# Kernel tuning notes

Measured on AMD Instinct MI355X. Metric: run time of the kernel, lower is better.

The kernel has to match this reference:

```python
import jax, jax.numpy as jnp
import numpy as np

B, H, T, K, V = 2, 8, 2048, 128, 128


def setup_inputs() -> dict:
    key = jax.random.key(0)
    k1, k2, k3, k4, k5 = jax.random.split(key, 5)
    return {
        "q": jax.random.normal(k1, (B, H, T, K), dtype=jnp.float32),
        "k": jax.random.normal(k2, (B, H, T, K), dtype=jnp.float32),
        "v": jax.random.normal(k3, (B, H, T, V), dtype=jnp.float32),
        "i_gate": jax.random.normal(k4, (B, H, T), dtype=jnp.float32),
        "f_gate": jax.random.normal(k5, (B, H, T), dtype=jnp.float32),
    }


def reference(q, k, v, i_gate, f_gate):
    # Stabilized parallel mLSTM (same math as the chunked Triton kernel,
    # expressed in natural-log base instead of base-2).
    Bq, Hq, Tq, Kd = q.shape
    scale = Kd ** -0.5
    logf = jax.nn.log_sigmoid(f_gate)                      # [B,H,T]
    fc = jnp.cumsum(logf, axis=-1)                         # cumulative forget logits
    # log decay matrix: logD[t,s] = i[s] + (fc[t] - fc[s]) for s <= t
    logD = fc[..., :, None] - fc[..., None, :] + i_gate[..., None, :]  # [B,H,T,T]
    mask = jnp.tril(jnp.ones((Tq, Tq), dtype=bool))
    logD_masked = jnp.where(mask, logD, -jnp.inf)
    m = jnp.max(logD_masked, axis=-1)                      # row-wise stabilizer [B,H,T]
    D = jnp.where(mask, jnp.exp(logD - m[..., None]), 0.0) # stabilized decay matrix
    S = jnp.einsum("bhtk,bhsk->bhts", q, k) * scale * D    # gated scores
    norm = jnp.maximum(jnp.abs(jnp.sum(S, axis=-1)), jnp.exp(-m))  # [B,H,T]
    h = jnp.einsum("bhts,bhsv->bhtv", S, v) / norm[..., None]
    return h
```

## Files before the change

kernel.cpp:

```cpp
#include <hip/hip_runtime.h>

#define T_SEQ 2048
#define DHEAD 128
#define NBH 16
#define SCALE 0.08838834764831845f

typedef unsigned short u16;
typedef unsigned int u32;
typedef u16 u16x4 __attribute__((ext_vector_type(4)));
typedef u16 u16x8 __attribute__((ext_vector_type(8)));
typedef u32 u32x2 __attribute__((ext_vector_type(2)));
typedef short s16x4 __attribute__((ext_vector_type(4)));
typedef __bf16 bf16x8 __attribute__((ext_vector_type(8)));
typedef float f32x4 __attribute__((ext_vector_type(4)));

__device__ __forceinline__ u16 f2bfu(float x) {
  union { float f; unsigned u; } c; c.f = x;
  unsigned u = c.u;
  u = u + 0x7FFFu + ((u >> 16) & 1u);
  return (u16)(u >> 16);
}

__device__ __forceinline__ bf16x8 ldsFrag(const u16* p) {
  u16x8 t = *(const u16x8*)p;
  return __builtin_bit_cast(bf16x8, t);
}

__device__ __forceinline__ f32x4 mfma16x16x16bf16(s16x4 a, s16x4 b, f32x4 c) {
#if __has_builtin(__builtin_amdgcn_mfma_f32_16x16x16bf16_1k)
  return __builtin_amdgcn_mfma_f32_16x16x16bf16_1k(a, b, c, 0, 0, 0);
#else
  asm("v_mfma_f32_16x16x16_bf16 %0, %1, %2, %0" : "+v"(c) : "v"(a), "v"(b));
  return c;
#endif
}

__global__ __launch_bounds__(1024) void gate_scan_kernel(
    const float* __restrict__ ig, const float* __restrict__ fg,
    float* __restrict__ a_out, float* __restrict__ c_out,
    float* __restrict__ fc_out)
{
  const int bh = blockIdx.x, tid = threadIdx.x;
  const int w = tid >> 6, lane = tid & 63;
  const int base = bh * T_SEQ + tid * 2;
  __shared__ float wsum[16];
  __shared__ float wmax[16];

  const float x0 = fg[base], x1 = fg[base + 1];
  const float ls0 = fminf(x0, 0.f) - log1pf(expf(-fabsf(x0)));
  const float ls1 = fminf(x1, 0.f) - log1pf(expf(-fabsf(x1)));
  const float s = ls0 + ls1;

  float sc = s;
#pragma unroll
  for (int off = 1; off < 64; off <<= 1) {
    const float t = __shfl_up(sc, off, 64);
    if (lane >= off) sc += t;
  }
  if (lane == 63) wsum[w] = sc;
  __syncthreads();
  float wo = 0.f;
#pragma unroll
  for (int i = 0; i < 15; ++i) if (i < w) wo += wsum[i];
  const float excl = wo + (sc - s);
  const float fc0 = excl + ls0;
  const float fc1 = excl + ls0 + ls1;
  fc_out[base] = fc0; fc_out[base + 1] = fc1;
  const float a0 = ig[base] - fc0;
  const float a1 = ig[base + 1] - fc1;
  a_out[base] = a0; a_out[base + 1] = a1;

  const float m = fmaxf(a0, a1);
  float mc = m;
#pragma unroll
  for (int off = 1; off < 64; off <<= 1) {
    const float t = __shfl_up(mc, off, 64);
    if (lane >= off) mc = fmaxf(mc, t);
  }
  if (lane == 63) wmax[w] = mc;
  __syncthreads();
  float wmo = -INFINITY;
#pragma unroll
  for (int i = 0; i < 15; ++i) if (i < w) wmo = fmaxf(wmo, wmax[i]);
  const float prev = __shfl_up(mc, 1, 64);
  float exclm = (lane > 0) ? prev : -INFINITY;
  exclm = fmaxf(exclm, wmo);
  c_out[base] = fmaxf(exclm, a0);
  c_out[base + 1] = fmaxf(exclm, m);
}

__global__ __launch_bounds__(256) void cvt_kv_kernel(
    const float* __restrict__ kk, const float* __restrict__ v,
    const float* __restrict__ ag, const float* __restrict__ cg,
    u16* __restrict__ kbf, u16* __restrict__ vt)
{
  const int bh = blockIdx.y, kt = blockIdx.x, tid = threadIdx.x;
  {
    const int r = tid >> 2;
    const int c0 = (tid & 3) * 32;
    const int row = kt * 64 + r;
    const float sc = __expf(ag[bh * T_SEQ + row] - cg[bh * T_SEQ + (row | 63)]);
    const float* sp = kk + ((size_t)bh * T_SEQ + row) * DHEAD + c0;
    u16* dp = kbf + ((size_t)bh * T_SEQ + row) * DHEAD + c0;
#pragma unroll
    for (int j = 0; j < 8; ++j) {
      const float4 x = *(const float4*)(sp + j * 4);
      u16x4 pq;
      pq[0] = f2bfu(x.x * sc); pq[1] = f2bfu(x.y * sc);
      pq[2] = f2bfu(x.z * sc); pq[3] = f2bfu(x.w * sc);
      *(u16x4*)(dp + j * 4) = pq;
    }
  }
  __shared__ __align__(16) u16 L[128 * 72];
  const int n0 = (tid & 31) * 4, k0 = (tid >> 5) * 8;
  const float* vp = v + ((size_t)bh * T_SEQ + kt * 64 + k0) * DHEAD + n0;
  u16 tv[4][8];
#pragma unroll
  for (int rr = 0; rr < 8; ++rr) {
    const float4 x = *(const float4*)(vp + rr * DHEAD);
    tv[0][rr] = f2bfu(x.x); tv[1][rr] = f2bfu(x.y);
    tv[2][rr] = f2bfu(x.z); tv[3][rr] = f2bfu(x.w);
  }
#pragma unroll
  for (int j = 0; j < 4; ++j) {
    u16x8 pq;
#pragma unroll
    for (int rr = 0; rr < 8; ++rr) pq[rr] = tv[j][rr];
    *(u16x8*)(&L[(n0 + j) * 72 + k0]) = pq;
  }
  __syncthreads();
  const int row = tid >> 1, s0 = (tid & 1) * 32;
  u16* op = vt + ((size_t)bh * DHEAD + row) * T_SEQ + kt * 64 + s0;
#pragma unroll
  for (int i = 0; i < 4; ++i)
    *(u16x8*)(op + i * 8) = *(const u16x8*)(&L[row * 72 + s0 + i * 8]);
}

template <bool FAST>
__global__ __launch_bounds__(1024, 4) void mlstm_fwd_kernel(
    const float* __restrict__ qg, const float* __restrict__ kxg,
    const float* __restrict__ vg,
    const u16* __restrict__ kbf, const u16* __restrict__ vtbf,
    const float* __restrict__ ag, const float* __restrict__ cg,
    const float* __restrict__ fcg, float* __restrict__ out)
{
  const int bx = (int)blockIdx.x;
  const int bh = bx & 15, p = bx >> 4;
  const int tid = (int)threadIdx.x;
  const int w = tid >> 6, lane = tid & 63;
  const int quad = lane >> 4, l16 = lane & 15;
  const int kg = w & 3, rq = w >> 2;

  const int qtA = 31 - p, qtB = p;
  const int nA = qtA + 1;

  __shared__ __align__(16) unsigned char SM[100352];
  u16* Kst = (u16*)SM;
  float* osh = (float*)(SM + 65536);
  float* rsh = (float*)(SM + 99328);

  const size_t hoff = (size_t)bh * T_SEQ * DHEAD;
  const int goff = bh * T_SEQ;

  bf16x8 qf[4];
  auto loadQ = [&](int lqt) {
    const float* qp = qg + hoff + (size_t)(lqt * 64 + rq * 16 + l16) * DHEAD + quad * 8;
#pragma unroll
    for (int kc = 0; kc < 4; ++kc) {
      const float4 x0 = *(const float4*)(qp + kc * 32);
      const float4 x1 = *(const float4*)(qp + kc * 32 + 4);
      u16x8 t;
      t[0] = f2bfu(x0.x); t[1] = f2bfu(x0.y); t[2] = f2bfu(x0.z); t[3] = f2bfu(x0.w);
      t[4] = f2bfu(x1.x); t[5] = f2bfu(x1.y); t[6] = f2bfu(x1.z); t[7] = f2bfu(x1.w);
      qf[kc] = __builtin_bit_cast(bf16x8, t);
    }
  };

  f32x4 oa[8];
  float rsacc;
  auto zeroAcc = [&]() {
#pragma unroll
    for (int mt = 0; mt < 8; ++mt) oa[mt] = (f32x4){0.f, 0.f, 0.f, 0.f};
    rsacc = 0.f;
  };
  zeroAcc();

  const int skey = tid >> 4, sdb = (tid & 15) ^ (skey & 7);
  const u16* ksBase = kbf + (size_t)goff * DHEAD + (size_t)skey * DHEAD + sdb * 8;
  const int svn = tid >> 3, svk = (tid & 7) ^ (svn & 7);
  const u16* vsBase = vtbf + (size_t)bh * DHEAD * T_SEQ + (size_t)svn * T_SEQ + svk * 8;

  auto stp = [&](int s) { return s < nA ? s : s - nA; };

  auto ld = [&](int s, u16x8& kr, u16x8& vr) {
    if (FAST) {
      const int st = stp(s);
      kr = *(const u16x8*)(ksBase + (size_t)st * 64 * DHEAD);
      vr = *(const u16x8*)(vsBase + st * 64);
    }
  };
  auto wr = [&](int s, u16x8 kr, u16x8 vr, u16* KbL) {
    if (FAST) {
      *(u16x8*)(KbL + tid * 8) = kr;
      *(u16x8*)(KbL + 8192 + tid * 8) = vr;
    } else {
      const int st = stp(s);
      const float ct = cg[goff + st * 64 + 63];
      const float* kp = kxg + hoff + (size_t)(st * 64 + skey) * DHEAD + sdb * 8;
      const float* vp = vg + hoff + (size_t)(st * 64) * DHEAD;
      const float scv = __expf(ag[goff + st * 64 + skey] - ct);
      const float4 x0 = *(const float4*)kp;
      const float4 x1 = *(const float4*)(kp + 4);
      u16x8 pk;
      pk[0] = f2bfu(x0.x * scv); pk[1] = f2bfu(x0.y * scv);
      pk[2] = f2bfu(x0.z * scv); pk[3] = f2bfu(x0.w * scv);
      pk[4] = f2bfu(x1.x * scv); pk[5] = f2bfu(x1.y * scv);
      pk[6] = f2bfu(x1.z * scv); pk[7] = f2bfu(x1.w * scv);
      *(u16x8*)(KbL + tid * 8) = pk;
      u16x8 pw;
#pragma unroll
      for (int rr = 0; rr < 8; ++rr)
        pw[rr] = f2bfu(vp[(size_t)(svk * 8 + rr) * DHEAD + svn]);
      *(u16x8*)(KbL + 8192 + tid * 8) = pw;
    }
  };

  const int keyA = kg * 16 + l16;
  const int ksw  = l16 & 7;
  const int vbase = l16 * 64 + (((kg * 2 + (quad >> 1)) ^ (l16 & 7)) * 8) + (quad & 1) * 4;

  auto computeStage = [&](int cqt, int st, const u16* KbL, float ccmax) {
    const u16* VbL = KbL + 8192;

    f32x4 sa = (f32x4){0.f, 0.f, 0.f, 0.f};
#pragma unroll
    for (int kc = 0; kc < 4; ++kc) {
      const bf16x8 kf = ldsFrag(KbL + keyA * 128 + (((kc * 4 + quad) ^ ksw) * 8));
      sa = __builtin_amdgcn_mfma_f32_16x16x32_bf16(kf, qf[kc], sa, 0, 0, 0);
    }

    const float etile = SCALE * __expf(cg[goff + st * 64 + 63] - ccmax);
    float x0 = sa[0] * etile, x1 = sa[1] * etile;
    float x2 = sa[2] * etile, x3 = sa[3] * etile;
    if (st == cqt) {
      const int qr = rq * 16 + l16, kb0 = kg * 16 + quad * 4;
      if (kb0 + 0 > qr) x0 = 0.f;
      if (kb0 + 1 > qr) x1 = 0.f;
      if (kb0 + 2 > qr) x2 = 0.f;
      if (kb0 + 3 > qr) x3 = 0.f;
    }
    rsacc += (x0 + x1) + (x2 + x3);
    u32 plo, phi;
    asm("v_cvt_pk_bf16_f32 %0, %1, %2" : "=v"(plo) : "v"(x0), "v"(x1));
    asm("v_cvt_pk_bf16_f32 %0, %1, %2" : "=v"(phi) : "v"(x2), "v"(x3));
    const s16x4 pfr = __builtin_bit_cast(s16x4, (u32x2){plo, phi});

#pragma unroll
    for (int mt = 0; mt < 8; ++mt) {
      const s16x4 va = *(const s16x4*)(VbL + vbase + mt * 1024);
      oa[mt] = mfma16x16x16bf16(va, pfr, oa[mt]);
    }
  };

  auto epilogue = [&](int eqt, float ecmax) {
    float x = rsacc;
    x += __shfl_xor(x, 16, 64);
    x += __shfl_xor(x, 32, 64);
    if (lane < 16) rsh[kg * 64 + rq * 16 + lane] = x;
    __syncthreads();
    float inv = 0.f;
    if (kg == 3) {
      const int row = rq * 16 + l16;
      const float tot = rsh[row] + rsh[64 + row] + rsh[128 + row] + rsh[192 + row];
      const float nf = __expf(-(ecmax + fcg[goff + eqt * 64 + row]));
      inv = 1.f / fmaxf(fabsf(tot), nf);
    }
    for (int r = 0; r < 4; ++r) {
      if (kg == r) {
        const int row = rq * 16 + l16;
#pragma unroll
        for (int mt = 0; mt < 8; ++mt) {
          float* ap = osh + row * 132 + mt * 16 + quad * 4;
          f32x4 vv = oa[mt];
          if (r > 0) vv = vv + *(const f32x4*)ap;
          if (r == 3) vv = vv * inv;
          *(f32x4*)ap = vv;
        }
      }
      __syncthreads();
    }
    const int col = tid & 31, r0 = tid >> 5;
#pragma unroll
    for (int i = 0; i < 2; ++i) {
      const int row = r0 + 32 * i;
      const f32x4 vv = *(const f32x4*)(osh + row * 132 + col * 4);
      *(f32x4*)(out + hoff + (size_t)(eqt * 64 + row) * DHEAD + col * 4) = vv;
    }
    __syncthreads();
  };

  int qt = qtA;
  float cmax = cg[goff + qtA * 64 + 63];
  loadQ(qtA);
  u16x8 k0, v0, k1, v1;
  ld(0, k0, v0);
  wr(0, k0, v0, Kst);
  ld(1, k1, v1);
  __syncthreads();

  auto maybeTransition = [&](int it) {
    if (it == nA - 1) {
      loadQ(qtB);
      epilogue(qtA, cmax);
      zeroAcc();
      qt = qtB;
      cmax = cg[goff + qtB * 64 + 63];
    }
  };

  for (int g = 0; g < 17; ++g) {
    {
      const int it = 2 * g;
      if (it < 32) wr(it + 1, k1, v1, Kst + 16384);
      if (it + 2 < 33) ld(it + 2, k0, v0);
      computeStage(qt, stp(it), Kst, cmax);
      __syncthreads();
      maybeTransition(it);
    }
    if (2 * g + 1 < 33) {
      const int it = 2 * g + 1;
      if (it < 32) wr(it + 1, k0, v0, Kst);
      if (it + 2 < 33) ld(it + 2, k1, v1);
      computeStage(qt, stp(it), Kst + 16384, cmax);
      __syncthreads();
      maybeTransition(it);
    }
  }
  epilogue(qtB, cmax);
}

extern "C" void kernel_launch(void* const* d_in, const int* in_sizes, int n_in,
                              void* d_out, int out_size, void* d_ws, size_t ws_size,
                              hipStream_t stream) {
  const float* q  = (const float*)d_in[0];
  const float* k  = (const float*)d_in[1];
  const float* v  = (const float*)d_in[2];
  const float* ig = (const float*)d_in[3];
  const float* fg = (const float*)d_in[4];

  const size_t gate_bytes = (size_t)3 * NBH * T_SEQ * sizeof(float);
  const size_t kv_elems   = (size_t)NBH * T_SEQ * DHEAD;
  const bool fast = ws_size >= gate_bytes + 2 * kv_elems * sizeof(u16);

  float* a_ws  = (float*)d_ws;
  float* c_ws  = a_ws + NBH * T_SEQ;
  float* fc_ws = c_ws + NBH * T_SEQ;
  u16* kbf  = (u16*)((char*)d_ws + gate_bytes);
  u16* vtbf = kbf + kv_elems;

  gate_scan_kernel<<<dim3(NBH), dim3(1024), 0, stream>>>(ig, fg, a_ws, c_ws, fc_ws);
  if (fast) {
    cvt_kv_kernel<<<dim3(T_SEQ / 64, NBH), dim3(256), 0, stream>>>(
        k, v, a_ws, c_ws, kbf, vtbf);
    mlstm_fwd_kernel<true><<<dim3(256), dim3(1024), 0, stream>>>(
        q, k, v, kbf, vtbf, a_ws, c_ws, fc_ws, (float*)d_out);
  } else {
    mlstm_fwd_kernel<false><<<dim3(256), dim3(1024), 0, stream>>>(
        q, k, v, kbf, vtbf, a_ws, c_ws, fc_ws, (float*)d_out);
  }
}
```

Measured before the change: 148.1 us.

## Fuse gate scan and K/V conversion into main kernel via cooperative grid sync

Merges the three launches (gate scan, K/V bf16 conversion, attention) into one cooperative kernel. Each block recomputes its head's gate scan into shared memory, converts two K/V tiles, then all blocks wait at a grid-wide barrier before the attention phase. Gate values are now read from LDS or via lane shuffles instead of from global memory. This removes two launch gaps and the global gate traffic, but every block repeats the scan redundantly and pays for a grid barrier. The cooperative launch also requires all 256 blocks of 1024 threads with about 118 KB of LDS each to be resident at once.

Result: slower. 197.1 us (+33.1%).

```diff
diff --git a/kernel.cpp b/kernel.cpp
--- a/kernel.cpp
+++ b/kernel.cpp
@@ -1,9 +1,12 @@
 #include <hip/hip_runtime.h>
+#include <hip/hip_cooperative_groups.h>
 
 #define T_SEQ 2048
 #define DHEAD 128
 #define NBH 16
 #define SCALE 0.08838834764831845f
+
+namespace cg = cooperative_groups;
 
 typedef unsigned short u16;
 typedef unsigned int u32;
@@ -35,114 +38,12 @@
 #endif
 }
 
-__global__ __launch_bounds__(1024) void gate_scan_kernel(
-    const float* __restrict__ ig, const float* __restrict__ fg,
-    float* __restrict__ a_out, float* __restrict__ c_out,
-    float* __restrict__ fc_out)
-{
-  const int bh = blockIdx.x, tid = threadIdx.x;
-  const int w = tid >> 6, lane = tid & 63;
-  const int base = bh * T_SEQ + tid * 2;
-  __shared__ float wsum[16];
-  __shared__ float wmax[16];
-
-  const float x0 = fg[base], x1 = fg[base + 1];
-  const float ls0 = fminf(x0, 0.f) - log1pf(expf(-fabsf(x0)));
-  const float ls1 = fminf(x1, 0.f) - log1pf(expf(-fabsf(x1)));
-  const float s = ls0 + ls1;
-
-  float sc = s;
-#pragma unroll
-  for (int off = 1; off < 64; off <<= 1) {
-    const float t = __shfl_up(sc, off, 64);
-    if (lane >= off) sc += t;
-  }
-  if (lane == 63) wsum[w] = sc;
-  __syncthreads();
-  float wo = 0.f;
-#pragma unroll
-  for (int i = 0; i < 15; ++i) if (i < w) wo += wsum[i];
-  const float excl = wo + (sc - s);
-  const float fc0 = excl + ls0;
-  const float fc1 = excl + ls0 + ls1;
-  fc_out[base] = fc0; fc_out[base + 1] = fc1;
-  const float a0 = ig[base] - fc0;
-  const float a1 = ig[base + 1] - fc1;
-  a_out[base] = a0; a_out[base + 1] = a1;
-
-  const float m = fmaxf(a0, a1);
-  float mc = m;
-#pragma unroll
-  for (int off = 1; off < 64; off <<= 1) {
-    const float t = __shfl_up(mc, off, 64);
-    if (lane >= off) mc = fmaxf(mc, t);
-  }
-  if (lane == 63) wmax[w] = mc;
-  __syncthreads();
-  float wmo = -INFINITY;
-#pragma unroll
-  for (int i = 0; i < 15; ++i) if (i < w) wmo = fmaxf(wmo, wmax[i]);
-  const float prev = __shfl_up(mc, 1, 64);
-  float exclm = (lane > 0) ? prev : -INFINITY;
-  exclm = fmaxf(exclm, wmo);
-  c_out[base] = fmaxf(exclm, a0);
-  c_out[base + 1] = fmaxf(exclm, m);
-}
-
-__global__ __launch_bounds__(256) void cvt_kv_kernel(
-    const float* __restrict__ kk, const float* __restrict__ v,
-    const float* __restrict__ ag, const float* __restrict__ cg,
-    u16* __restrict__ kbf, u16* __restrict__ vt)
-{
-  const int bh = blockIdx.y, kt = blockIdx.x, tid = threadIdx.x;
-  {
-    const int r = tid >> 2;
-    const int c0 = (tid & 3) * 32;
-    const int row = kt * 64 + r;
-    const float sc = __expf(ag[bh * T_SEQ + row] - cg[bh * T_SEQ + (row | 63)]);
-    const float* sp = kk + ((size_t)bh * T_SEQ + row) * DHEAD + c0;
-    u16* dp = kbf + ((size_t)bh * T_SEQ + row) * DHEAD + c0;
-#pragma unroll
-    for (int j = 0; j < 8; ++j) {
-      const float4 x = *(const float4*)(sp + j * 4);
-      u16x4 pq;
-      pq[0] = f2bfu(x.x * sc); pq[1] = f2bfu(x.y * sc);
-      pq[2] = f2bfu(x.z * sc); pq[3] = f2bfu(x.w * sc);
-      *(u16x4*)(dp + j * 4) = pq;
-    }
-  }
-  __shared__ __align__(16) u16 L[128 * 72];
-  const int n0 = (tid & 31) * 4, k0 = (tid >> 5) * 8;
-  const float* vp = v + ((size_t)bh * T_SEQ + kt * 64 + k0) * DHEAD + n0;
-  u16 tv[4][8];
-#pragma unroll
-  for (int rr = 0; rr < 8; ++rr) {
-    const float4 x = *(const float4*)(vp + rr * DHEAD);
-    tv[0][rr] = f2bfu(x.x); tv[1][rr] = f2bfu(x.y);
-    tv[2][rr] = f2bfu(x.z); tv[3][rr] = f2bfu(x.w);
-  }
-#pragma unroll
-  for (int j = 0; j < 4; ++j) {
-    u16x8 pq;
-#pragma unroll
-    for (int rr = 0; rr < 8; ++rr) pq[rr] = tv[j][rr];
-    *(u16x8*)(&L[(n0 + j) * 72 + k0]) = pq;
-  }
-  __syncthreads();
-  const int row = tid >> 1, s0 = (tid & 1) * 32;
-  u16* op = vt + ((size_t)bh * DHEAD + row) * T_SEQ + kt * 64 + s0;
-#pragma unroll
-  for (int i = 0; i < 4; ++i)
-    *(u16x8*)(op + i * 8) = *(const u16x8*)(&L[row * 72 + s0 + i * 8]);
-}
-
 template <bool FAST>
-__global__ __launch_bounds__(1024, 4) void mlstm_fwd_kernel(
+__global__ __launch_bounds__(1024, 4) void mlstm_fused_kernel(
     const float* __restrict__ qg, const float* __restrict__ kxg,
-    const float* __restrict__ vg,
-    const u16* __restrict__ kbf, const u16* __restrict__ vtbf,
-    const float* __restrict__ ag, const float* __restrict__ cg,
-    const float* __restrict__ fcg, float* __restrict__ out)
+    const float* __restrict__ vg, const float* __restrict__ ig,
+    const float* __restrict__ fg, u16* __restrict__ kbf,
+    u16* __restrict__ vtbf, float* __restrict__ out)
 {
   const int bx = (int)blockIdx.x;
   const int bh = bx & 15, p = bx >> 4;
@@ -154,13 +55,97 @@
   const int qtA = 31 - p, qtB = p;
   const int nA = qtA + 1;
 
-  __shared__ __align__(16) unsigned char SM[100352];
+  __shared__ __align__(16) unsigned char SM[117888];
   u16* Kst = (u16*)SM;
-  float* osh = (float*)(SM + 65536);
-  float* rsh = (float*)(SM + 99328);
+  float* osh  = (float*)(SM + 65536);
+  float* rsh  = (float*)(SM + 99328);
+  float* ash  = (float*)(SM + 101376);
+  float* fsh  = (float*)(SM + 109568);
+  float* cend = (float*)(SM + 117760);
 
   const size_t hoff = (size_t)bh * T_SEQ * DHEAD;
-  const int goff = bh * T_SEQ;
+
+  {
+    float* wsum = rsh;
+    float* wmax = rsh + 16;
+    const int gbase = bh * T_SEQ + tid * 2;
+
+    const float x0 = fg[gbase], x1 = fg[gbase + 1];
+    const float ls0 = fminf(x0, 0.f) - log1pf(expf(-fabsf(x0)));
+    const float ls1 = fminf(x1, 0.f) - log1pf(expf(-fabsf(x1)));
+    const float s = ls0 + ls1;
+
+    float sc = s;
+#pragma unroll
+    for (int off = 1; off < 64; off <<= 1) {
+      const float t = __shfl_up(sc, off, 64);
+      if (lane >= off) sc += t;
+    }
+    if (lane == 63) wsum[w] = sc;
+    __syncthreads();
+    float wo = 0.f;
+#pragma unroll
+    for (int i = 0; i < 15; ++i) if (i < w) wo += wsum[i];
+    const float excl = wo + (sc - s);
+    const float fc0 = excl + ls0;
+    const float fc1 = excl + ls0 + ls1;
+    fsh[tid * 2] = fc0; fsh[tid * 2 + 1] = fc1;
+    const float a0 = ig[gbase] - fc0;
+    const float a1 = ig[gbase + 1] - fc1;
+    ash[tid * 2] = a0; ash[tid * 2 + 1] = a1;
+
+    const float m = fmaxf(a0, a1);
+    float mc = m;
+#pragma unroll
+    for (int off = 1; off < 64; off <<= 1) {
+      const float t = __shfl_up(mc, off, 64);
+      if (lane >= off) mc = fmaxf(mc, t);
+    }
+    if (lane == 63) wmax[w] = mc;
+    __syncthreads();
+    float wmo = -INFINITY;
+#pragma unroll
+    for (int i = 0; i < 15; ++i) if (i < w) wmo = fmaxf(wmo, wmax[i]);
+    const float prev = __shfl_up(mc, 1, 64);
+    float exclm = (lane > 0) ? prev : -INFINITY;
+    exclm = fmaxf(exclm, wmo);
+    const float c1v = fmaxf(exclm, m);
+    if ((tid & 31) == 31) cend[(tid * 2 + 1) >> 6] = c1v;
+    __syncthreads();
+  }
+
+  if (FAST) {
+#pragma unroll
+    for (int t = 0; t < 2; ++t) {
+      const int kt = 2 * p + t;
+      {
+        const int r = tid >> 4, ci = (tid & 15) * 8;
+        const int row = kt * 64 + r;
+        const float sc = __expf(ash[row] - cend[kt]);
+        const float* sp = kxg + hoff + (size_t)row * DHEAD + ci;
+        const float4 x0 = *(const float4*)sp;
+        const float4 x1 = *(const float4*)(sp + 4);
+        u16x8 pk;
+        pk[0] = f2bfu(x0.x * sc); pk[1] = f2bfu(x0.y * sc);
+        pk[2] = f2bfu(x0.z * sc); pk[3] = f2bfu(x0.w * sc);
+        pk[4] = f2bfu(x1.x * sc); pk[5] = f2bfu(x1.y * sc);
+        pk[6] = f2bfu(x1.z * sc); pk[7] = f2bfu(x1.w * sc);
+        *(u16x8*)(kbf + hoff + (size_t)row * DHEAD + ci) = pk;
+      }
+      {
+        const int n = tid & 127, kb = tid >> 7;
+        const float* vp = vg + hoff + (size_t)(kt * 64 + kb * 8) * DHEAD + n;
+        u16x8 pw;
+#pragma unroll
+        for (int r8 = 0; r8 < 8; ++r8) pw[r8] = f2bfu(vp[(size_t)r8 * DHEAD]);
+        *(u16x8*)(vtbf + (size_t)bh * DHEAD * T_SEQ + (size_t)n * T_SEQ
+                  + kt * 64 + kb * 8) = pw;
+      }
+    }
+    cg::this_grid().sync();
+  }
+
+  const float cglr = cend[lane & 31];
 
   bf16x8 qf[4];
   auto loadQ = [&](int lqt) {
@@ -186,7 +171,7 @@
   zeroAcc();
 
   const int skey = tid >> 4, sdb = (tid & 15) ^ (skey & 7);
-  const u16* ksBase = kbf + (size_t)goff * DHEAD + (size_t)skey * DHEAD + sdb * 8;
+  const u16* ksBase = kbf + hoff + (size_t)skey * DHEAD + sdb * 8;
   const int svn = tid >> 3, svk = (tid & 7) ^ (svn & 7);
   const u16* vsBase = vtbf + (size_t)bh * DHEAD * T_SEQ + (size_t)svn * T_SEQ + svk * 8;
 
@@ -205,10 +190,10 @@
       *(u16x8*)(KbL + 8192 + tid * 8) = vr;
     } else {
       const int st = stp(s);
-      const float ct = cg[goff + st * 64 + 63];
+      const float ct = cend[st];
       const float* kp = kxg + hoff + (size_t)(st * 64 + skey) * DHEAD + sdb * 8;
       const float* vp = vg + hoff + (size_t)(st * 64) * DHEAD;
-      const float scv = __expf(ag[goff + st * 64 + skey] - ct);
+      const float scv = __expf(ash[st * 64 + skey] - ct);
       const float4 x0 = *(const float4*)kp;
       const float4 x1 = *(const float4*)(kp + 4);
       u16x8 pk;
@@ -239,7 +224,7 @@
       sa = __builtin_amdgcn_mfma_f32_16x16x32_bf16(kf, qf[kc], sa, 0, 0, 0);
     }
 
-    const float etile = SCALE * __expf(cg[goff + st * 64 + 63] - ccmax);
+    const float etile = SCALE * __expf(__shfl(cglr, st, 64) - ccmax);
     float x0 = sa[0] * etile, x1 = sa[1] * etile;
     float x2 = sa[2] * etile, x3 = sa[3] * etile;
     if (st == cqt) {
@@ -272,7 +257,7 @@
     if (kg == 3) {
       const int row = rq * 16 + l16;
       const float tot = rsh[row] + rsh[64 + row] + rsh[128 + row] + rsh[192 + row];
-      const float nf = __expf(-(ecmax + fcg[goff + eqt * 64 + row]));
+      const float nf = __expf(-(ecmax + fsh[eqt * 64 + row]));
       inv = 1.f / fmaxf(fabsf(tot), nf);
     }
     for (int r = 0; r < 4; ++r) {
@@ -300,7 +285,7 @@
   };
 
   int qt = qtA;
-  float cmax = cg[goff + qtA * 64 + 63];
+  float cmax = __shfl(cglr, qtA, 64);
   loadQ(qtA);
   u16x8 k0, v0, k1, v1;
   ld(0, k0, v0);
@@ -314,7 +299,7 @@
       epilogue(qtA, cmax);
       zeroAcc();
       qt = qtB;
-      cmax = cg[goff + qtB * 64 + 63];
+      cmax = __shfl(cglr, qtB, 64);
     }
   };
 
@@ -348,24 +333,21 @@
   const float* ig = (const float*)d_in[3];
   const float* fg = (const float*)d_in[4];
 
-  const size_t gate_bytes = (size_t)3 * NBH * T_SEQ * sizeof(float);
-  const size_t kv_elems   = (size_t)NBH * T_SEQ * DHEAD;
-  const bool fast = ws_size >= gate_bytes + 2 * kv_elems * sizeof(u16);
-
-  float* a_ws  = (float*)d_ws;
-  float* c_ws  = a_ws + NBH * T_SEQ;
-  float* fc_ws = c_ws + NBH * T_SEQ;
-  u16* kbf  = (u16*)((char*)d_ws + gate_bytes);
+  const size_t kv_elems = (size_t)NBH * T_SEQ * DHEAD;
+  const bool fast = ws_size >= 2 * kv_elems * sizeof(u16);
+
+  u16* kbf  = (u16*)d_ws;
   u16* vtbf = kbf + kv_elems;
-
-  gate_scan_kernel<<<dim3(NBH), dim3(1024), 0, stream>>>(ig, fg, a_ws, c_ws, fc_ws);
+  float* outp = (float*)d_out;
+
   if (fast) {
-    cvt_kv_kernel<<<dim3(T_SEQ / 64, NBH), dim3(256), 0, stream>>>(
-        k, v, a_ws, c_ws, kbf, vtbf);
-    mlstm_fwd_kernel<true><<<dim3(256), dim3(1024), 0, stream>>>(
-        q, k, v, kbf, vtbf, a_ws, c_ws, fc_ws, (float*)d_out);
+    void* args[] = {(void*)&q, (void*)&k, (void*)&v, (void*)&ig, (void*)&fg,
+                    (void*)&kbf, (void*)&vtbf, (void*)&outp};
+    hipLaunchCooperativeKernel(
+        reinterpret_cast<void*>(mlstm_fused_kernel<true>),
+        dim3(256), dim3(1024), args, 0, stream);
   } else {
-    mlstm_fwd_kernel<false><<<dim3(256), dim3(1024), 0, stream>>>(
-        q, k, v, kbf, vtbf, a_ws, c_ws, fc_ws, (float*)d_out);
+    mlstm_fused_kernel<false><<<dim3(256), dim3(1024), 0, stream>>>(
+        q, k, v, ig, fg, kbf, vtbf, outp);
   }
 }
```
